# Optimization experiments

Hardware: AMD Instinct MI355X
Metric: run time of the kernel (lower is better)

## Reference

```python
import jax, jax.numpy as jnp
import numpy as np

NUM_NODES = 100000
NUM_EDGES = 1200000
DIM = 64
NUM_LAYERS = 3
NUM_GRAPHS = 512
BN_EPS = 1e-5


def setup_inputs() -> dict:
    key = jax.random.key(0)
    ks = jax.random.split(key, 12)
    x = jax.random.normal(ks[0], (NUM_NODES, DIM), dtype=jnp.float32)
    edge_index = jax.random.randint(ks[1], (2, NUM_EDGES), 0, NUM_NODES, dtype=jnp.int64)
    edge_weight = jax.random.uniform(ks[2], (NUM_EDGES,), dtype=jnp.float32)
    batch = jnp.sort(jax.random.randint(ks[3], (NUM_NODES,), 0, NUM_GRAPHS, dtype=jnp.int64))
    W1 = jax.random.normal(ks[4], (NUM_LAYERS, DIM, DIM), dtype=jnp.float32) * 0.1
    b1 = jax.random.normal(ks[5], (NUM_LAYERS, DIM), dtype=jnp.float32) * 0.1
    W2 = jax.random.normal(ks[6], (NUM_LAYERS, DIM, DIM), dtype=jnp.float32) * 0.1
    b2 = jax.random.normal(ks[7], (NUM_LAYERS, DIM), dtype=jnp.float32) * 0.1
    gamma = jax.random.uniform(ks[8], (NUM_LAYERS, DIM), dtype=jnp.float32) + 0.5
    beta = jax.random.normal(ks[9], (NUM_LAYERS, DIM), dtype=jnp.float32) * 0.1
    return {"x": x, "edge_index": edge_index, "edge_weight": edge_weight,
            "batch": batch, "pool": 0, "W1": W1, "b1": b1, "W2": W2,
            "b2": b2, "gamma": gamma, "beta": beta}


def reference(x, edge_index, edge_weight, batch, pool, W1, b1, W2, b2, gamma, beta):
    # WGINConv (eps=0): h = MLP(x + scatter_add(edge_weight * x[src] -> dst))
    # then ReLU, then BatchNorm1d in training mode (batch statistics).
    src, dst = edge_index[0], edge_index[1]
    n_nodes = x.shape[0]
    xs = []
    for i in range(W1.shape[0]):
        msg = x[src] * edge_weight[:, None]                       # [E, D] gather
        agg = jax.ops.segment_sum(msg, dst, num_segments=n_nodes)  # [N, D] scatter-add
        h = agg + x                                                # (1+eps)*x, eps=0
        h = jax.nn.relu(h @ W1[i].T + b1[i]) @ W2[i].T + b2[i]     # GIN MLP
        h = jax.nn.relu(h)
        mu = h.mean(0)
        var = ((h - mu) ** 2).mean(0)                              # biased var (BN train)
        x = gamma[i] * (h - mu) * jax.lax.rsqrt(var + BN_EPS) + beta[i]
        xs.append(x)
    if pool == 0:  # 'add' pooling (static python int)
        xpool = [jax.ops.segment_sum(v, batch, num_segments=NUM_GRAPHS) for v in xs]
    else:          # 'mean' pooling
        counts = jax.ops.segment_sum(jnp.ones((n_nodes,), x.dtype), batch,
                                     num_segments=NUM_GRAPHS)
        denom = jnp.maximum(counts, 1.0)[:, None]
        xpool = [jax.ops.segment_sum(v, batch, num_segments=NUM_GRAPHS) / denom for v in xs]
    return (jnp.concatenate(xpool, axis=1), jnp.concatenate(xs, axis=1))
```

## Files before the change

kernel.cpp:

```cpp
#include <hip/hip_runtime.h>

#define N_NODES 100000
#define N_EDGES 1200000
#define DIM     64
#define N_LAYERS 3
#define N_GRAPHS 512
#define OUTD    192
#define BN_EPS  1e-5f

#define NPB 64
#define LDS_PITCH 65
#define NLBLK ((N_NODES + NPB - 1) / NPB)

#define BSHIFT 9
#define BUCK_NODES (1 << BSHIFT)
#define NBUK ((N_NODES + BUCK_NODES - 1) / BUCK_NODES)
#define EPB 4096
#define NPBLK ((N_EDGES + EPB - 1) / EPB)

__device__ __forceinline__ unsigned short f2bf(float f) {
    unsigned u = __float_as_uint(f);
    return (unsigned short)((u + 0x7FFFu + ((u >> 16) & 1u)) >> 16);
}
__device__ __forceinline__ float bf2f(unsigned short h) {
    return __uint_as_float(((unsigned)h) << 16);
}

__global__ void transpose_w(const float* __restrict__ W1, const float* __restrict__ W2,
                            float* __restrict__ W1T, float* __restrict__ W2T,
                            float* __restrict__ idaff) {
    int idx = blockIdx.x * blockDim.x + threadIdx.x;
    if (idx < 128) idaff[idx] = (idx < 64) ? 1.0f : 0.0f;
    if (idx >= N_LAYERS * DIM * DIM) return;
    int l = idx >> 12;
    int r = idx & 4095;
    int j = r >> 6;
    int k = r & 63;
    int dstp = (l << 12) + k * DIM + j;
    W1T[dstp] = W1[idx];
    W2T[dstp] = W2[idx];
}

__global__ void __launch_bounds__(256) to_bf16(const float* __restrict__ x,
                                               unsigned short* __restrict__ x16) {
    int i = blockIdx.x * blockDim.x + threadIdx.x;
    if (i >= N_NODES * 16) return;
    float4 v = ((const float4*)x)[i];
    ushort4 r;
    r.x = f2bf(v.x); r.y = f2bf(v.y); r.z = f2bf(v.z); r.w = f2bf(v.w);
    ((ushort4*)x16)[i] = r;
}

__global__ void __launch_bounds__(256) part_hist(const int* __restrict__ dst,
                                                 int* __restrict__ hist,
                                                 int* __restrict__ tot) {
    __shared__ int h[NBUK];
    int t = threadIdx.x;
    if (t < NBUK) h[t] = 0;
    __syncthreads();
    int base = blockIdx.x * EPB;
    for (int i = t; i < EPB; i += 256) {
        int e = base + i;
        if (e < N_EDGES) atomicAdd(&h[dst[e] >> BSHIFT], 1);
    }
    __syncthreads();
    if (t < NBUK) {
        int v = h[t];
        hist[blockIdx.x * NBUK + t] = v;
        if (v) atomicAdd(&tot[t], v);
    }
}

__global__ void __launch_bounds__(256) scan196(const int* __restrict__ tot,
                                               int* __restrict__ bstart) {
    __shared__ int lds[256];
    int t = threadIdx.x;
    int v = (t < NBUK) ? tot[t] : 0;
    lds[t] = v;
    __syncthreads();
    for (int o = 1; o < 256; o <<= 1) {
        int add = (t >= o) ? lds[t - o] : 0;
        __syncthreads();
        lds[t] += add;
        __syncthreads();
    }
    if (t < NBUK) bstart[t] = lds[t] - v;
    if (t == 0) bstart[NBUK] = N_EDGES;
}

__global__ void __launch_bounds__(256) base_fill(const int* __restrict__ hist,
                                                 const int* __restrict__ bstart,
                                                 int* __restrict__ base) {
    __shared__ int c[512];
    __shared__ int ssum[256];
    int b = blockIdx.x, t = threadIdx.x;
    c[t] = (t < NPBLK) ? hist[t * NBUK + b] : 0;
    c[t + 256] = (t + 256 < NPBLK) ? hist[(t + 256) * NBUK + b] : 0;
    __syncthreads();
    int c0 = c[2 * t], c1 = c[2 * t + 1];
    int ps = c0 + c1;
    ssum[t] = ps;
    __syncthreads();
    int v = ps;
    for (int o = 1; o < 256; o <<= 1) {
        int add = (t >= o) ? ssum[t - o] : 0;
        __syncthreads();
        ssum[t] += add;
        __syncthreads();
    }
    int excl = ssum[t] - v + bstart[b];
    if (2 * t < NPBLK)     base[(2 * t) * NBUK + b] = excl;
    if (2 * t + 1 < NPBLK) base[(2 * t + 1) * NBUK + b] = excl + c0;
}

__global__ void __launch_bounds__(256) part_scatter(
        const int* __restrict__ src, const int* __restrict__ dst,
        const float* __restrict__ ew, const int* __restrict__ base,
        int2* __restrict__ pp) {
    __shared__ int cur[NBUK];
    int t = threadIdx.x;
    if (t < NBUK) cur[t] = base[blockIdx.x * NBUK + t];
    __syncthreads();
    int bb = blockIdx.x * EPB;
    for (int i = t; i < EPB; i += 256) {
        int e = bb + i;
        if (e < N_EDGES) {
            int d = dst[e];
            int bk = d >> BSHIFT;
            int pos = atomicAdd(&cur[bk], 1);
            int dl = d & (BUCK_NODES - 1);
            pp[pos] = make_int2(src[e] | (dl << 17), __float_as_int(ew[e]));
        }
    }
}

__global__ void __launch_bounds__(256) csr_build(
        const int2* __restrict__ pp, const int* __restrict__ bstart,
        int* __restrict__ seg, int2* __restrict__ pe) {
    __shared__ int cnt[BUCK_NODES];
    __shared__ int ssum[256];
    int b = blockIdx.x, t = threadIdx.x;
    int ebeg = bstart[b], eend = bstart[b + 1];
    cnt[t] = 0;
    cnt[t + 256] = 0;
    __syncthreads();
    for (int e = ebeg + t; e < eend; e += 256)
        atomicAdd(&cnt[pp[e].x >> 17], 1);
    __syncthreads();
    int c0 = cnt[2 * t], c1 = cnt[2 * t + 1];
    int ps = c0 + c1;
    ssum[t] = ps;
    __syncthreads();
    int v = ps;
    for (int o = 1; o < 256; o <<= 1) {
        int add = (t >= o) ? ssum[t - o] : 0;
        __syncthreads();
        ssum[t] += add;
        __syncthreads();
    }
    int excl = ssum[t] - v;
    int o0 = ebeg + excl;
    int o1 = o0 + c0;
    int n0 = (b << BSHIFT) + 2 * t;
    if (n0 < N_NODES) seg[n0] = o0;
    if (n0 + 1 < N_NODES) seg[n0 + 1] = o1;
    __syncthreads();
    cnt[2 * t] = o0;
    cnt[2 * t + 1] = o1;
    __syncthreads();
    for (int e = ebeg + t; e < eend; e += 256) {
        int2 p = pp[e];
        int pos = atomicAdd(&cnt[p.x >> 17], 1);
        pe[pos] = make_int2(p.x & 0x1FFFF, p.y);
    }
    if (b == 0 && t == 0) seg[N_NODES] = N_EDGES;
}

__global__ void __launch_bounds__(256) layer_kernel(
    const float* __restrict__ x_in, int xstride,
    const unsigned short* __restrict__ x16in,
    unsigned short* __restrict__ x16out, int wr16,
    const int* __restrict__ seg,
    const int2* __restrict__ pe,
    const float* __restrict__ affine ,
    const float* __restrict__ W1T, const float* __restrict__ b1,
    const float* __restrict__ W2T, const float* __restrict__ b2,
    float* __restrict__ out ,
    float* __restrict__ pstat ) {
    __shared__ float lds[NPB * LDS_PITCH];
    int t = threadIdx.x;
    int lane = t & 63;
    int wid = __builtin_amdgcn_readfirstlane(t >> 6);
    int nbase = blockIdx.x * NPB;

    int slot = lane >> 4;
    int col  = lane & 15;
    const float4* aff4 = (const float4*)affine;
    float4 sc4 = aff4[col];
    float4 sh4 = aff4[16 + col];

    for (int nn = 0; nn < 16; ++nn) {
        int nl = wid * 16 + nn;
        int n = nbase + nl;
        float ax = 0.f, ay = 0.f, az = 0.f, aw = 0.f, wsa = 0.f;
        float bx = 0.f, by = 0.f, bz = 0.f, bw = 0.f, wsb = 0.f;
        if (n < N_NODES) {
            int beg = seg[n];
            int end = seg[n + 1];
#define GBODY(EI, X, Y, Z, W, WS)                                              \
            if ((EI) < end) {                                                  \
                int2 p = pe[EI];                                               \
                float w = __int_as_float(p.y);                                 \
                ushort4 hv =                                                   \
                    ((const ushort4*)(x16in + (size_t)p.x * DIM))[col];        \
                X = fmaf(w, bf2f(hv.x), X); Y = fmaf(w, bf2f(hv.y), Y);        \
                Z = fmaf(w, bf2f(hv.z), Z); W = fmaf(w, bf2f(hv.w), W);        \
                WS += w;                                                       \
            }
            for (int e = beg; e < end; e += 16) {
                int e0 = e + slot;
                GBODY(e0,      ax, ay, az, aw, wsa)
                GBODY(e0 + 4,  bx, by, bz, bw, wsb)
                GBODY(e0 + 8,  ax, ay, az, aw, wsa)
                GBODY(e0 + 12, bx, by, bz, bw, wsb)
            }
#undef GBODY
        }
        float sx = ax + bx, sy = ay + by, sz = az + bz, sw = aw + bw;
        float ws = wsa + wsb;
        sx += __shfl_xor(sx, 16); sy += __shfl_xor(sy, 16);
        sz += __shfl_xor(sz, 16); sw += __shfl_xor(sw, 16);
        ws += __shfl_xor(ws, 16);
        sx += __shfl_xor(sx, 32); sy += __shfl_xor(sy, 32);
        sz += __shfl_xor(sz, 32); sw += __shfl_xor(sw, 32);
        ws += __shfl_xor(ws, 32);
        if (lane < 16) {
            float r0 = 0.f, r1 = 0.f, r2 = 0.f, r3 = 0.f;
            if (n < N_NODES) {
                const float4* xr =
                    (const float4*)(x_in + (size_t)n * xstride) + col;
                float4 s = *xr;
                float shw = 1.0f + ws;
                r0 = fmaf(sc4.x, sx + s.x, sh4.x * shw);
                r1 = fmaf(sc4.y, sy + s.y, sh4.y * shw);
                r2 = fmaf(sc4.z, sz + s.z, sh4.z * shw);
                r3 = fmaf(sc4.w, sw + s.w, sh4.w * shw);
            }
            int lb = nl * LDS_PITCH + col * 4;
            lds[lb] = r0; lds[lb + 1] = r1; lds[lb + 2] = r2; lds[lb + 3] = r3;
        }
    }
    __syncthreads();

    float h[16];
#pragma unroll
    for (int jj = 0; jj < 16; ++jj) h[jj] = b1[wid * 16 + jj];
#pragma unroll 4
    for (int k = 0; k < DIM; ++k) {
        float xv = lds[lane * LDS_PITCH + k];
        const float* wr = W1T + k * DIM + wid * 16;
#pragma unroll
        for (int jj = 0; jj < 16; ++jj) h[jj] = fmaf(xv, wr[jj], h[jj]);
    }
#pragma unroll
    for (int jj = 0; jj < 16; ++jj) h[jj] = fmaxf(h[jj], 0.0f);
    __syncthreads();
#pragma unroll
    for (int jj = 0; jj < 16; ++jj) lds[lane * LDS_PITCH + wid * 16 + jj] = h[jj];
    __syncthreads();

    float o[16];
#pragma unroll
    for (int jj = 0; jj < 16; ++jj) o[jj] = b2[wid * 16 + jj];
#pragma unroll 4
    for (int k = 0; k < DIM; ++k) {
        float hv = lds[lane * LDS_PITCH + k];
        const float* wr = W2T + k * DIM + wid * 16;
#pragma unroll
        for (int jj = 0; jj < 16; ++jj) o[jj] = fmaf(hv, wr[jj], o[jj]);
    }
    int n = nbase + lane;
    bool valid = (n < N_NODES);
#pragma unroll
    for (int jj = 0; jj < 16; ++jj) o[jj] = fmaxf(o[jj], 0.0f);
    if (valid) {
        float* orow = out + (size_t)n * OUTD + wid * 16;
#pragma unroll
        for (int jj = 0; jj < 16; jj += 4) {
            *(float4*)(orow + jj) = make_float4(o[jj], o[jj + 1], o[jj + 2], o[jj + 3]);
        }
        if (wr16) {
            unsigned short* hrow = x16out + (size_t)n * DIM + wid * 16;
#pragma unroll
            for (int jj = 0; jj < 16; jj += 4) {
                ushort4 hq;
                hq.x = f2bf(o[jj]);     hq.y = f2bf(o[jj + 1]);
                hq.z = f2bf(o[jj + 2]); hq.w = f2bf(o[jj + 3]);
                *(ushort4*)(hrow + jj) = hq;
            }
        }
    }

    float my_s = 0.0f, my_q = 0.0f;
#pragma unroll
    for (int jj = 0; jj < 16; ++jj) {
        float v = valid ? o[jj] : 0.0f;
        float vs = v, vq = v * v;
#pragma unroll
        for (int m = 1; m < 64; m <<= 1) {
            vs += __shfl_xor(vs, m);
            vq += __shfl_xor(vq, m);
        }
        if (lane == jj) { my_s = vs; my_q = vq; }
    }
    if (lane < 16) {
        size_t base = (size_t)blockIdx.x * 128 + wid * 16 + lane;
        pstat[base] = my_s;
        pstat[base + 64] = my_q;
    }
}

__global__ void __launch_bounds__(256) reduce_stats(
    const float* __restrict__ pstat,
    const float* __restrict__ gamma, const float* __restrict__ beta,
    float* __restrict__ ss ) {
    __shared__ double part[16][16];
    int b = blockIdx.x;
    int t = threadIdx.x;
    int slot = t & 15;
    int g = t >> 4;
    int d = b * 8 + (slot & 7);
    int off = (slot < 8) ? 0 : 64;
    double s = 0.0;
    for (int blk = g; blk < NLBLK; blk += 16)
        s += (double)pstat[(size_t)blk * 128 + off + d];
    part[g][slot] = s;
    __syncthreads();
    if (t < 16) {
        double x = 0.0;
#pragma unroll
        for (int k = 0; k < 16; ++k) x += part[k][t];
        part[0][t] = x;
    }
    __syncthreads();
    if (t < 8) {
        int dd = b * 8 + t;
        double mu = part[0][t] / (double)N_NODES;
        double var = part[0][8 + t] / (double)N_NODES - mu * mu;
        float inv = (float)(1.0 / sqrt(var + (double)BN_EPS));
        float sc = gamma[dd] * inv;
        ss[dd] = sc;
        ss[64 + dd] = beta[dd] - (float)mu * sc;
    }
}

__global__ void bn_pool(float* __restrict__ xs,
                        const int* __restrict__ batch,
                        const float* __restrict__ ss ,
                        float* __restrict__ pooled) {
    int g = blockIdx.x;
    int part = blockIdx.y;
    int d = threadIdx.x;
    int l = d >> 6, dd = d & 63;
    float sc = ss[l * 128 + dd];
    float sh = ss[l * 128 + 64 + dd];
    int start, end;
    {
        int lo = 0, hi = N_NODES;
        while (lo < hi) { int m = (lo + hi) >> 1; if (batch[m] < g) lo = m + 1; else hi = m; }
        start = lo;
    }
    {
        int lo = start, hi = N_NODES;
        while (lo < hi) { int m = (lo + hi) >> 1; if (batch[m] <= g) lo = m + 1; else hi = m; }
        end = lo;
    }
    float acc = 0.0f;
    for (int n = start + part; n < end; n += 4) {
        float* p = xs + (size_t)n * OUTD + d;
        float v = fmaf(*p, sc, sh);
        *p = v;
        acc += v;
    }
    atomicAdd(&pooled[(size_t)g * OUTD + d], acc);
}

extern "C" void kernel_launch(void* const* d_in, const int* in_sizes, int n_in,
                              void* d_out, int out_size, void* d_ws, size_t ws_size,
                              hipStream_t stream) {
    const float* x0    = (const float*)d_in[0];
    const int*   ei    = (const int*)d_in[1];
    const float* ew    = (const float*)d_in[2];
    const int*   batch = (const int*)d_in[3];
    const float* W1    = (const float*)d_in[5];
    const float* b1    = (const float*)d_in[6];
    const float* W2    = (const float*)d_in[7];
    const float* b2    = (const float*)d_in[8];
    const float* gamma = (const float*)d_in[9];
    const float* beta  = (const float*)d_in[10];

    float* pooled = (float*)d_out;
    float* xs     = pooled + (size_t)N_GRAPHS * OUTD;

    const int* src = ei;
    const int* dst = ei + N_EDGES;

    int2*  pe     = (int2*)d_ws;
    int*   seg    = (int*)(pe + N_EDGES);
    int*   tot    = seg + N_NODES + 4;
    int*   bstart = tot + NBUK + 4;
    float* W1T    = (float*)(bstart + NBUK + 4);
    float* W2T    = W1T + N_LAYERS * DIM * DIM;
    float* idaff  = W2T + N_LAYERS * DIM * DIM;
    float* ss     = idaff + 128;
    float* pstat  = ss + N_LAYERS * 128;
    char* uni = (char*)(pstat + (size_t)NLBLK * 128);
    int2*  pp     = (int2*)uni;
    int*   hist   = (int*)(pp + N_EDGES);
    int*   pbase  = hist + (size_t)NPBLK * NBUK;
    unsigned short* x16a = (unsigned short*)uni;
    unsigned short* x16b = x16a + (size_t)N_NODES * DIM;

    transpose_w<<<(N_LAYERS * DIM * DIM + 255) / 256, 256, 0, stream>>>(
        W1, W2, W1T, W2T, idaff);

    hipMemsetAsync(tot, 0, (NBUK + 4) * sizeof(int), stream);
    part_hist<<<NPBLK, 256, 0, stream>>>(dst, hist, tot);
    scan196<<<1, 256, 0, stream>>>(tot, bstart);
    base_fill<<<NBUK, 256, 0, stream>>>(hist, bstart, pbase);
    part_scatter<<<NPBLK, 256, 0, stream>>>(src, dst, ew, pbase, pp);
    csr_build<<<NBUK, 256, 0, stream>>>(pp, bstart, seg, pe);

    to_bf16<<<(N_NODES * 16 + 255) / 256, 256, 0, stream>>>(x0, x16a);

    for (int i = 0; i < N_LAYERS; ++i) {
        const float* xin = (i == 0) ? x0 : (xs + (size_t)(i - 1) * DIM);
        int xstride = (i == 0) ? DIM : OUTD;
        const float* affine = (i == 0) ? idaff : (ss + (size_t)(i - 1) * 128);
        const unsigned short* x16in = (i == 1) ? x16b : x16a;
        unsigned short* x16out = (i == 0) ? x16b : x16a;
        int wr16 = (i < N_LAYERS - 1) ? 1 : 0;

        layer_kernel<<<NLBLK, 256, 0, stream>>>(
            xin, xstride, x16in, x16out, wr16, seg, pe, affine,
            W1T + (size_t)i * DIM * DIM, b1 + (size_t)i * DIM,
            W2T + (size_t)i * DIM * DIM, b2 + (size_t)i * DIM,
            xs + (size_t)i * DIM, pstat);

        reduce_stats<<<8, 256, 0, stream>>>(
            pstat, gamma + (size_t)i * DIM, beta + (size_t)i * DIM,
            ss + (size_t)i * 128);
    }

    hipMemsetAsync(pooled, 0, (size_t)N_GRAPHS * OUTD * sizeof(float), stream);
    dim3 pgrid(N_GRAPHS, 4);
    bn_pool<<<pgrid, OUTD, 0, stream>>>(xs, batch, ss, pooled);
}
```

Before: 539.4 us.

## Fuse CSR build into one persistent kernel with grid barriers; drop bf16 prepass

The five CSR-construction launches (histogram, scan, base fill, partition scatter, per-bucket CSR) become a single 256-block kernel that synchronises through a software grid barrier. The separate fp32-to-bf16 conversion is removed: layer 0 now gathers fp32 rows directly through a templated layer kernel. The pooled-output memset moves into the last reduce_stats launch. This cuts launch count and small-kernel gaps, but relies on all 256 blocks being co-resident for the spin barrier, and fewer, larger blocks do the edge binning.

New measurement: 644.2 us. 1.19x slower.

```diff
diff --git a/kernel.cpp b/kernel.cpp
--- a/kernel.cpp
+++ b/kernel.cpp
@@ -15,8 +15,8 @@
 #define BSHIFT 9
 #define BUCK_NODES (1 << BSHIFT)
 #define NBUK ((N_NODES + BUCK_NODES - 1) / BUCK_NODES)
-#define EPB 4096
-#define NPBLK ((N_EDGES + EPB - 1) / EPB)
+#define NBLK2 256
+#define EPB2 ((N_EDGES + NBLK2 - 1) / NBLK2)
 
 __device__ __forceinline__ unsigned short f2bf(float f) {
     unsigned u = __float_as_uint(f);
@@ -26,11 +26,31 @@
     return __uint_as_float(((unsigned)h) << 16);
 }
 
+__device__ __forceinline__ void gbar(int* bc) {
+    __syncthreads();
+    if (threadIdx.x == 0) {
+        int g = __hip_atomic_load(&bc[1], __ATOMIC_RELAXED, __HIP_MEMORY_SCOPE_AGENT);
+        __threadfence();
+        int a = __hip_atomic_fetch_add(&bc[0], 1, __ATOMIC_ACQ_REL, __HIP_MEMORY_SCOPE_AGENT);
+        if (a == NBLK2 - 1) {
+            __hip_atomic_store(&bc[0], 0, __ATOMIC_RELAXED, __HIP_MEMORY_SCOPE_AGENT);
+            __hip_atomic_store(&bc[1], g + 1, __ATOMIC_RELEASE, __HIP_MEMORY_SCOPE_AGENT);
+        } else {
+            while (__hip_atomic_load(&bc[1], __ATOMIC_ACQUIRE, __HIP_MEMORY_SCOPE_AGENT) <= g) {
+                __builtin_amdgcn_s_sleep(2);
+            }
+        }
+        __threadfence();
+    }
+    __syncthreads();
+}
+
 __global__ void transpose_w(const float* __restrict__ W1, const float* __restrict__ W2,
                             float* __restrict__ W1T, float* __restrict__ W2T,
-                            float* __restrict__ idaff) {
+                            float* __restrict__ idaff, int* __restrict__ barcnt) {
     int idx = blockIdx.x * blockDim.x + threadIdx.x;
     if (idx < 128) idaff[idx] = (idx < 64) ? 1.0f : 0.0f;
+    if (idx < 2) barcnt[idx] = 0;
     if (idx >= N_LAYERS * DIM * DIM) return;
     int l = idx >> 12;
     int r = idx & 4095;
@@ -41,141 +61,112 @@
     W2T[dstp] = W2[idx];
 }
 
-__global__ void __launch_bounds__(256) to_bf16(const float* __restrict__ x,
-                                               unsigned short* __restrict__ x16) {
-    int i = blockIdx.x * blockDim.x + threadIdx.x;
-    if (i >= N_NODES * 16) return;
-    float4 v = ((const float4*)x)[i];
-    ushort4 r;
-    r.x = f2bf(v.x); r.y = f2bf(v.y); r.z = f2bf(v.z); r.w = f2bf(v.w);
-    ((ushort4*)x16)[i] = r;
-}
-
-__global__ void __launch_bounds__(256) part_hist(const int* __restrict__ dst,
-                                                 int* __restrict__ hist,
-                                                 int* __restrict__ tot) {
-    __shared__ int h[NBUK];
-    int t = threadIdx.x;
-    if (t < NBUK) h[t] = 0;
-    __syncthreads();
-    int base = blockIdx.x * EPB;
-    for (int i = t; i < EPB; i += 256) {
-        int e = base + i;
-        if (e < N_EDGES) atomicAdd(&h[dst[e] >> BSHIFT], 1);
-    }
-    __syncthreads();
-    if (t < NBUK) {
-        int v = h[t];
-        hist[blockIdx.x * NBUK + t] = v;
-        if (v) atomicAdd(&tot[t], v);
-    }
-}
-
-__global__ void __launch_bounds__(256) scan196(const int* __restrict__ tot,
-                                               int* __restrict__ bstart) {
-    __shared__ int lds[256];
-    int t = threadIdx.x;
-    int v = (t < NBUK) ? tot[t] : 0;
-    lds[t] = v;
-    __syncthreads();
-    for (int o = 1; o < 256; o <<= 1) {
-        int add = (t >= o) ? lds[t - o] : 0;
-        __syncthreads();
-        lds[t] += add;
-        __syncthreads();
-    }
-    if (t < NBUK) bstart[t] = lds[t] - v;
-    if (t == 0) bstart[NBUK] = N_EDGES;
-}
-
-__global__ void __launch_bounds__(256) base_fill(const int* __restrict__ hist,
-                                                 const int* __restrict__ bstart,
-                                                 int* __restrict__ base) {
-    __shared__ int c[512];
-    __shared__ int ssum[256];
-    int b = blockIdx.x, t = threadIdx.x;
-    c[t] = (t < NPBLK) ? hist[t * NBUK + b] : 0;
-    c[t + 256] = (t + 256 < NPBLK) ? hist[(t + 256) * NBUK + b] : 0;
-    __syncthreads();
-    int c0 = c[2 * t], c1 = c[2 * t + 1];
-    int ps = c0 + c1;
-    ssum[t] = ps;
-    __syncthreads();
-    int v = ps;
-    for (int o = 1; o < 256; o <<= 1) {
-        int add = (t >= o) ? ssum[t - o] : 0;
-        __syncthreads();
-        ssum[t] += add;
-        __syncthreads();
-    }
-    int excl = ssum[t] - v + bstart[b];
-    if (2 * t < NPBLK)     base[(2 * t) * NBUK + b] = excl;
-    if (2 * t + 1 < NPBLK) base[(2 * t + 1) * NBUK + b] = excl + c0;
-}
-
-__global__ void __launch_bounds__(256) part_scatter(
+__global__ void __launch_bounds__(256) bin_all(
         const int* __restrict__ src, const int* __restrict__ dst,
-        const float* __restrict__ ew, const int* __restrict__ base,
-        int2* __restrict__ pp) {
-    __shared__ int cur[NBUK];
-    int t = threadIdx.x;
-    if (t < NBUK) cur[t] = base[blockIdx.x * NBUK + t];
-    __syncthreads();
-    int bb = blockIdx.x * EPB;
-    for (int i = t; i < EPB; i += 256) {
-        int e = bb + i;
-        if (e < N_EDGES) {
+        const float* __restrict__ ew,
+        int* __restrict__ hist,
+        int* __restrict__ pbase,
+        int* __restrict__ colsum,
+        int2* __restrict__ pp, int* __restrict__ seg, int2* __restrict__ pe,
+        int* __restrict__ barcnt) {
+    __shared__ int sA[512];
+    __shared__ int sB[256];
+    __shared__ int sC[256];
+    int k = blockIdx.x, t = threadIdx.x;
+    int e0 = k * EPB2;
+    int e1 = e0 + EPB2; if (e1 > N_EDGES) e1 = N_EDGES;
+
+    if (t < NBUK) sB[t] = 0;
+    __syncthreads();
+    for (int e = e0 + t; e < e1; e += 256) atomicAdd(&sB[dst[e] >> BSHIFT], 1);
+    __syncthreads();
+    if (t < NBUK) hist[k * NBUK + t] = sB[t];
+    gbar(barcnt);
+
+    if (k < NBUK) {
+        int v = hist[t * NBUK + k];
+        sA[t] = v;
+        __syncthreads();
+        for (int o = 1; o < 256; o <<= 1) {
+            int add = (t >= o) ? sA[t - o] : 0;
+            __syncthreads();
+            sA[t] += add;
+            __syncthreads();
+        }
+        pbase[t * NBUK + k] = sA[t] - v;
+        if (t == 255) colsum[k] = sA[255];
+    }
+    gbar(barcnt);
+
+    {
+        int cs = (t < NBUK) ? colsum[t] : 0;
+        sA[t] = cs;
+        __syncthreads();
+        for (int o = 1; o < 256; o <<= 1) {
+            int add = (t >= o) ? sA[t - o] : 0;
+            __syncthreads();
+            sA[t] += add;
+            __syncthreads();
+        }
+        if (t < NBUK) sC[t] = sA[t] - cs + pbase[k * NBUK + t];
+        __syncthreads();
+        for (int e = e0 + t; e < e1; e += 256) {
             int d = dst[e];
             int bk = d >> BSHIFT;
-            int pos = atomicAdd(&cur[bk], 1);
-            int dl = d & (BUCK_NODES - 1);
-            pp[pos] = make_int2(src[e] | (dl << 17), __float_as_int(ew[e]));
-        }
-    }
-}
-
-__global__ void __launch_bounds__(256) csr_build(
-        const int2* __restrict__ pp, const int* __restrict__ bstart,
-        int* __restrict__ seg, int2* __restrict__ pe) {
-    __shared__ int cnt[BUCK_NODES];
-    __shared__ int ssum[256];
-    int b = blockIdx.x, t = threadIdx.x;
-    int ebeg = bstart[b], eend = bstart[b + 1];
-    cnt[t] = 0;
-    cnt[t + 256] = 0;
-    __syncthreads();
-    for (int e = ebeg + t; e < eend; e += 256)
-        atomicAdd(&cnt[pp[e].x >> 17], 1);
-    __syncthreads();
-    int c0 = cnt[2 * t], c1 = cnt[2 * t + 1];
-    int ps = c0 + c1;
-    ssum[t] = ps;
-    __syncthreads();
-    int v = ps;
-    for (int o = 1; o < 256; o <<= 1) {
-        int add = (t >= o) ? ssum[t - o] : 0;
-        __syncthreads();
-        ssum[t] += add;
-        __syncthreads();
-    }
-    int excl = ssum[t] - v;
-    int o0 = ebeg + excl;
-    int o1 = o0 + c0;
-    int n0 = (b << BSHIFT) + 2 * t;
-    if (n0 < N_NODES) seg[n0] = o0;
-    if (n0 + 1 < N_NODES) seg[n0 + 1] = o1;
-    __syncthreads();
-    cnt[2 * t] = o0;
-    cnt[2 * t + 1] = o1;
-    __syncthreads();
-    for (int e = ebeg + t; e < eend; e += 256) {
-        int2 p = pp[e];
-        int pos = atomicAdd(&cnt[p.x >> 17], 1);
-        pe[pos] = make_int2(p.x & 0x1FFFF, p.y);
-    }
-    if (b == 0 && t == 0) seg[N_NODES] = N_EDGES;
-}
-
+            int pos = atomicAdd(&sC[bk], 1);
+            pp[pos] = make_int2(src[e] | ((d & (BUCK_NODES - 1)) << 17),
+                                __float_as_int(ew[e]));
+        }
+    }
+    gbar(barcnt);
+
+    if (k < NBUK) {
+        int cs = (t < NBUK) ? colsum[t] : 0;
+        sB[t] = cs;
+        __syncthreads();
+        for (int o = 1; o < 256; o <<= 1) {
+            int add = (t >= o) ? sB[t - o] : 0;
+            __syncthreads();
+            sB[t] += add;
+            __syncthreads();
+        }
+        int eend = sB[k];
+        int ebeg = eend - colsum[k];
+        sA[t] = 0; sA[t + 256] = 0;
+        __syncthreads();
+        for (int e = ebeg + t; e < eend; e += 256)
+            atomicAdd(&sA[pp[e].x >> 17], 1);
+        __syncthreads();
+        int c0 = sA[2 * t], c1 = sA[2 * t + 1];
+        int ps = c0 + c1;
+        sC[t] = ps;
+        __syncthreads();
+        for (int o = 1; o < 256; o <<= 1) {
+            int add = (t >= o) ? sC[t - o] : 0;
+            __syncthreads();
+            sC[t] += add;
+            __syncthreads();
+        }
+        int excl = sC[t] - ps;
+        int o0 = ebeg + excl;
+        int o1 = o0 + c0;
+        int n0 = (k << BSHIFT) + 2 * t;
+        if (n0 < N_NODES) seg[n0] = o0;
+        if (n0 + 1 < N_NODES) seg[n0 + 1] = o1;
+        __syncthreads();
+        sA[2 * t] = o0;
+        sA[2 * t + 1] = o1;
+        __syncthreads();
+        for (int e = ebeg + t; e < eend; e += 256) {
+            int2 p = pp[e];
+            int pos = atomicAdd(&sA[p.x >> 17], 1);
+            pe[pos] = make_int2(p.x & 0x1FFFF, p.y);
+        }
+        if (k == 0 && t == 0) seg[N_NODES] = N_EDGES;
+    }
+}
+
+template <int BF16IN>
 __global__ void __launch_bounds__(256) layer_kernel(
     const float* __restrict__ x_in, int xstride,
     const unsigned short* __restrict__ x16in,
@@ -211,10 +202,19 @@
             if ((EI) < end) {                                                  \
                 int2 p = pe[EI];                                               \
                 float w = __int_as_float(p.y);                                 \
-                ushort4 hv =                                                   \
-                    ((const ushort4*)(x16in + (size_t)p.x * DIM))[col];        \
-                X = fmaf(w, bf2f(hv.x), X); Y = fmaf(w, bf2f(hv.y), Y);        \
-                Z = fmaf(w, bf2f(hv.z), Z); W = fmaf(w, bf2f(hv.w), W);        \
+                float vx, vy, vz, vw;                                          \
+                if (BF16IN) {                                                  \
+                    ushort4 hv =                                               \
+                        ((const ushort4*)(x16in + (size_t)p.x * DIM))[col];    \
+                    vx = bf2f(hv.x); vy = bf2f(hv.y);                          \
+                    vz = bf2f(hv.z); vw = bf2f(hv.w);                          \
+                } else {                                                       \
+                    float4 fv =                                                \
+                        ((const float4*)(x_in + (size_t)p.x * xstride))[col];  \
+                    vx = fv.x; vy = fv.y; vz = fv.z; vw = fv.w;                \
+                }                                                              \
+                X = fmaf(w, vx, X); Y = fmaf(w, vy, Y);                        \
+                Z = fmaf(w, vz, Z); W = fmaf(w, vw, W);                        \
                 WS += w;                                                       \
             }
             for (int e = beg; e < end; e += 16) {
@@ -323,10 +323,15 @@
 __global__ void __launch_bounds__(256) reduce_stats(
     const float* __restrict__ pstat,
     const float* __restrict__ gamma, const float* __restrict__ beta,
-    float* __restrict__ ss ) {
+    float* __restrict__ ss ,
+    float* __restrict__ pooled, int zpool) {
     __shared__ double part[16][16];
     int b = blockIdx.x;
     int t = threadIdx.x;
+    if (zpool) {
+        for (int i = b * 256 + t; i < N_GRAPHS * OUTD; i += 8 * 256)
+            pooled[i] = 0.0f;
+    }
     int slot = t & 15;
     int g = t >> 4;
     int d = b * 8 + (slot & 7);
@@ -407,9 +412,9 @@
 
     int2*  pe     = (int2*)d_ws;
     int*   seg    = (int*)(pe + N_EDGES);
-    int*   tot    = seg + N_NODES + 4;
-    int*   bstart = tot + NBUK + 4;
-    float* W1T    = (float*)(bstart + NBUK + 4);
+    int*   colsum = seg + N_NODES + 4;
+    int*   barcnt = colsum + NBUK + 4;
+    float* W1T    = (float*)(barcnt + 4);
     float* W2T    = W1T + N_LAYERS * DIM * DIM;
     float* idaff  = W2T + N_LAYERS * DIM * DIM;
     float* ss     = idaff + 128;
@@ -417,21 +422,15 @@
     char* uni = (char*)(pstat + (size_t)NLBLK * 128);
     int2*  pp     = (int2*)uni;
     int*   hist   = (int*)(pp + N_EDGES);
-    int*   pbase  = hist + (size_t)NPBLK * NBUK;
+    int*   pbase  = hist + (size_t)NBLK2 * NBUK;
     unsigned short* x16a = (unsigned short*)uni;
     unsigned short* x16b = x16a + (size_t)N_NODES * DIM;
 
     transpose_w<<<(N_LAYERS * DIM * DIM + 255) / 256, 256, 0, stream>>>(
-        W1, W2, W1T, W2T, idaff);
-
-    hipMemsetAsync(tot, 0, (NBUK + 4) * sizeof(int), stream);
-    part_hist<<<NPBLK, 256, 0, stream>>>(dst, hist, tot);
-    scan196<<<1, 256, 0, stream>>>(tot, bstart);
-    base_fill<<<NBUK, 256, 0, stream>>>(hist, bstart, pbase);
-    part_scatter<<<NPBLK, 256, 0, stream>>>(src, dst, ew, pbase, pp);
-    csr_build<<<NBUK, 256, 0, stream>>>(pp, bstart, seg, pe);
-
-    to_bf16<<<(N_NODES * 16 + 255) / 256, 256, 0, stream>>>(x0, x16a);
+        W1, W2, W1T, W2T, idaff, barcnt);
+
+    bin_all<<<NBLK2, 256, 0, stream>>>(src, dst, ew, hist, pbase, colsum,
+                                       pp, seg, pe, barcnt);
 
     for (int i = 0; i < N_LAYERS; ++i) {
         const float* xin = (i == 0) ? x0 : (xs + (size_t)(i - 1) * DIM);
@@ -441,18 +440,25 @@
         unsigned short* x16out = (i == 0) ? x16b : x16a;
         int wr16 = (i < N_LAYERS - 1) ? 1 : 0;
 
-        layer_kernel<<<NLBLK, 256, 0, stream>>>(
-            xin, xstride, x16in, x16out, wr16, seg, pe, affine,
-            W1T + (size_t)i * DIM * DIM, b1 + (size_t)i * DIM,
-            W2T + (size_t)i * DIM * DIM, b2 + (size_t)i * DIM,
-            xs + (size_t)i * DIM, pstat);
+        if (i == 0) {
+            layer_kernel<0><<<NLBLK, 256, 0, stream>>>(
+                xin, xstride, x16in, x16out, wr16, seg, pe, affine,
+                W1T + (size_t)i * DIM * DIM, b1 + (size_t)i * DIM,
+                W2T + (size_t)i * DIM * DIM, b2 + (size_t)i * DIM,
+                xs + (size_t)i * DIM, pstat);
+        } else {
+            layer_kernel<1><<<NLBLK, 256, 0, stream>>>(
+                xin, xstride, x16in, x16out, wr16, seg, pe, affine,
+                W1T + (size_t)i * DIM * DIM, b1 + (size_t)i * DIM,
+                W2T + (size_t)i * DIM * DIM, b2 + (size_t)i * DIM,
+                xs + (size_t)i * DIM, pstat);
+        }
 
         reduce_stats<<<8, 256, 0, stream>>>(
             pstat, gamma + (size_t)i * DIM, beta + (size_t)i * DIM,
-            ss + (size_t)i * 128);
-    }
-
-    hipMemsetAsync(pooled, 0, (size_t)N_GRAPHS * OUTD * sizeof(float), stream);
+            ss + (size_t)i * 128, pooled, (i == N_LAYERS - 1) ? 1 : 0);
+    }
+
     dim3 pgrid(N_GRAPHS, 4);
     bn_pool<<<pgrid, OUTD, 0, stream>>>(xs, batch, ss, pooled);
 }
```
